# Kernel optimization log

Measured on AMD Instinct MI355X. Metric: run time of the kernel, lower is better.

## Reference

```python
import jax, jax.numpy as jnp
import numpy as np

N_NODES = 100000
N_EDGES = 1600000
FEAT = 64
HEADS = 8
OUT_C = 8  # per-head out channels; HEADS*OUT_C == FEAT
BATCH = 64
MAXLEN = 2048
NEG_SLOPE = 0.2  # PyG GATConv default


def setup_inputs() -> dict:
    key = jax.random.key(0)
    ks = jax.random.split(key, 8)
    x = jax.random.normal(ks[0], (N_NODES, FEAT), dtype=jnp.float32)
    edge_index = jax.random.randint(ks[1], (2, N_EDGES), 0, N_NODES, dtype=jnp.int64)
    traj_seqs = jax.random.randint(ks[2], (BATCH, MAXLEN), 0, N_NODES, dtype=jnp.int64)
    seq_lengths = jax.random.randint(ks[3], (BATCH,), 1, MAXLEN, dtype=jnp.int64)
    # GATConv parameters (glorot-ish init)
    W = jax.random.normal(ks[4], (FEAT, HEADS * OUT_C), dtype=jnp.float32) * (1.0 / np.sqrt(FEAT))
    att_src = jax.random.normal(ks[5], (HEADS, OUT_C), dtype=jnp.float32) * 0.1
    att_dst = jax.random.normal(ks[6], (HEADS, OUT_C), dtype=jnp.float32) * 0.1
    bias = jnp.zeros((HEADS * OUT_C,), dtype=jnp.float32)
    return {"x": x, "W": W, "att_src": att_src, "att_dst": att_dst, "bias": bias,
            "edge_index": edge_index, "traj_seqs": traj_seqs, "seq_lengths": seq_lengths}


def reference(x, W, att_src, att_dst, bias, edge_index, traj_seqs, seq_lengths):
    N = x.shape[0]
    # PyG GATConv adds self loops by default
    loop = jnp.arange(N, dtype=edge_index.dtype)
    src = jnp.concatenate([edge_index[0], loop])  # message source j
    dst = jnp.concatenate([edge_index[1], loop])  # message target i

    xw = (x @ W).reshape(N, HEADS, OUT_C)              # [N,H,C]
    a_src = jnp.sum(xw * att_src, axis=-1)             # [N,H]
    a_dst = jnp.sum(xw * att_dst, axis=-1)             # [N,H]

    # edge attention logits and segment softmax over incoming edges of dst
    e = jax.nn.leaky_relu(a_src[src] + a_dst[dst], NEG_SLOPE)   # [E,H]
    m = jax.ops.segment_max(e, dst, num_segments=N)             # [N,H]
    m = jnp.where(jnp.isfinite(m), m, 0.0)
    ex = jnp.exp(e - m[dst])
    denom = jax.ops.segment_sum(ex, dst, num_segments=N)        # [N,H] (>0 via self loops)
    alpha = ex / denom[dst]                                     # [E,H]

    msg = alpha[:, :, None] * xw[src]                           # [E,H,C]
    out = jax.ops.segment_sum(msg, dst, num_segments=N)         # [N,H,C]
    node_emb = jax.nn.relu(out.reshape(N, HEADS * OUT_C) + bias)

    # batched gather into padded [B, maxlen, F] tensor, zero past seq_lengths
    emb = node_emb[traj_seqs]                                   # [B,L,F]
    mask = jnp.arange(traj_seqs.shape[1])[None, :] < seq_lengths[:, None]
    emb = emb * mask[:, :, None].astype(emb.dtype)
    return emb, seq_lengths
```

## Files before the change

kernel.cpp:

```cpp
#include <hip/hip_runtime.h>
#include <hip/hip_bf16.h>
#include <hip/hip_fp8.h>
#include <hip/hip_fp16.h>

#define N_NODESC 100000
#define N_EDGESC 1600000
#define FEATC 64
#define HEADSC 8
#define BATCHC 64
#define MAXLENC 2048
#define NBUCK 500
#define BSZ 200
#define CAP 6144
#define P3_EDGES 8192
#define K1B 391

__device__ __forceinline__ float b2f(unsigned short u){
  union { unsigned u; float f; } c; c.u = ((unsigned)u) << 16; return c.f;
}
__device__ __forceinline__ unsigned short f2b(float f){
  union { float f; unsigned u; } c; c.f = f;
  unsigned r = c.u + 0x7fffu + ((c.u >> 16) & 1u);
  return (unsigned short)(r >> 16);
}
__device__ __forceinline__ int clampi(int v, int lo, int hi){
  return v < lo ? lo : (v > hi ? hi : v);
}
__device__ __forceinline__ void unpack8(uint4 v, float* o){
  o[0] = b2f((unsigned short)(v.x & 0xffff)); o[1] = b2f((unsigned short)(v.x >> 16));
  o[2] = b2f((unsigned short)(v.y & 0xffff)); o[3] = b2f((unsigned short)(v.y >> 16));
  o[4] = b2f((unsigned short)(v.z & 0xffff)); o[5] = b2f((unsigned short)(v.z >> 16));
  o[6] = b2f((unsigned short)(v.w & 0xffff)); o[7] = b2f((unsigned short)(v.w >> 16));
}
__device__ __forceinline__ float fp8tof(unsigned char b){
  __hip_fp8_e4m3 q; q.__x = (__hip_fp8_storage_t)b; return (float)q;
}

__global__ __launch_bounds__(256) void k_pre(
    const unsigned short* __restrict__ x, const unsigned short* __restrict__ W,
    const unsigned short* __restrict__ attS, const unsigned short* __restrict__ attD,
    const int* __restrict__ ei,
    unsigned char* __restrict__ xw8, __half* __restrict__ a_srch,
    float* __restrict__ a_dst, int* __restrict__ cc)
{
  __shared__ float Wsf[64 * 64];
  __shared__ float as_s[64];
  __shared__ float ad_s[64];
  __shared__ int hh[NBUCK];
  int t = threadIdx.x;

  if (blockIdx.x >= K1B) {
    for (int i = t; i < NBUCK; i += 256) hh[i] = 0;
    __syncthreads();
    int g = (blockIdx.x - K1B) * 256 + t;
    if (g < N_EDGESC / 4) {
      int4 d = ((const int4*)(ei + N_EDGESC))[g];
      atomicAdd(&hh[clampi(d.x, 0, N_NODESC - 1) / BSZ], 1);
      atomicAdd(&hh[clampi(d.y, 0, N_NODESC - 1) / BSZ], 1);
      atomicAdd(&hh[clampi(d.z, 0, N_NODESC - 1) / BSZ], 1);
      atomicAdd(&hh[clampi(d.w, 0, N_NODESC - 1) / BSZ], 1);
    }
    __syncthreads();
    for (int i = t; i < NBUCK; i += 256) if (hh[i]) atomicAdd(&cc[i], hh[i]);
    return;
  }

  for (int i = t; i < 4096; i += 256) Wsf[i] = b2f(W[i]);
  if (t < 64) { as_s[t] = b2f(attS[t]); ad_s[t] = b2f(attD[t]); }
  __syncthreads();

  int g    = t & 3;
  int slot = t >> 2;
  int n0 = blockIdx.x * 256 + slot * 4;

  float acc[4][16];
  #pragma unroll
  for (int j = 0; j < 4; j++)
    #pragma unroll
    for (int c = 0; c < 16; c++) acc[j][c] = 0.f;

  const float4* Ws4 = (const float4*)Wsf;
  for (int i = 0; i < 8; i++) {
    float xu[4][8];
    #pragma unroll
    for (int j = 0; j < 4; j++) {
      int n = n0 + j;
      uint4 v = make_uint4(0u,0u,0u,0u);
      if (n < N_NODESC) v = ((const uint4*)(x + (size_t)n * 64))[i];
      unpack8(v, xu[j]);
    }
    #pragma unroll
    for (int u = 0; u < 8; u++) {
      int k = i * 8 + u;
      float4 w0 = Ws4[k * 16 + g * 4 + 0];
      float4 w1 = Ws4[k * 16 + g * 4 + 1];
      float4 w2 = Ws4[k * 16 + g * 4 + 2];
      float4 w3 = Ws4[k * 16 + g * 4 + 3];
      #pragma unroll
      for (int j = 0; j < 4; j++) {
        float xk = xu[j][u];
        acc[j][ 0] += xk * w0.x; acc[j][ 1] += xk * w0.y;
        acc[j][ 2] += xk * w0.z; acc[j][ 3] += xk * w0.w;
        acc[j][ 4] += xk * w1.x; acc[j][ 5] += xk * w1.y;
        acc[j][ 6] += xk * w1.z; acc[j][ 7] += xk * w1.w;
        acc[j][ 8] += xk * w2.x; acc[j][ 9] += xk * w2.y;
        acc[j][10] += xk * w2.z; acc[j][11] += xk * w2.w;
        acc[j][12] += xk * w3.x; acc[j][13] += xk * w3.y;
        acc[j][14] += xk * w3.z; acc[j][15] += xk * w3.w;
      }
    }
  }

  #pragma unroll
  for (int j = 0; j < 4; j++) {
    int n = n0 + j;
    if (n >= N_NODESC) break;
    union { unsigned u[4]; unsigned char b[16]; } pk;
    #pragma unroll
    for (int c = 0; c < 16; c++)
      pk.b[c] = (unsigned char)__hip_fp8_e4m3(acc[j][c]).__x;
    uint4 o; o.x = pk.u[0]; o.y = pk.u[1]; o.z = pk.u[2]; o.w = pk.u[3];
    *((uint4*)(xw8 + (size_t)n * 64 + g * 16)) = o;

    #pragma unroll
    for (int hl = 0; hl < 2; hl++) {
      int h = g * 2 + hl;
      float sa = 0.f, sd = 0.f;
      #pragma unroll
      for (int c = 0; c < 8; c++) {
        sa += acc[j][hl * 8 + c] * as_s[h * 8 + c];
        sd += acc[j][hl * 8 + c] * ad_s[h * 8 + c];
      }
      a_srch[n * 8 + h] = __float2half(sa);
      a_dst[n * 8 + h] = sd;
    }
  }
}

__global__ __launch_bounds__(1024) void k_csort(const int* __restrict__ ei,
                                                const int* __restrict__ cc,
                                                int* __restrict__ gcur,
                                                unsigned* __restrict__ cs) {
  __shared__ int bst[512];
  __shared__ int h[NBUCK], lst[NBUCK], lcur[NBUCK], gb[NBUCK];
  __shared__ int sc[512];
  __shared__ unsigned sorted[P3_EDGES];
  __shared__ unsigned short sbk[P3_EDGES];
  int t = threadIdx.x;
  int base = blockIdx.x * P3_EDGES;
  for (int i = t; i < NBUCK; i += 1024) h[i] = 0;
  int myc = 0;
  if (t < 512) { myc = (t < NBUCK) ? cc[t] : 0; bst[t] = myc; }
  __syncthreads();
  for (int off = 1; off < 512; off <<= 1) {
    int v = 0;
    if (t < 512) { v = bst[t]; if (t >= off) v += bst[t - off]; }
    __syncthreads();
    if (t < 512) bst[t] = v;
    __syncthreads();
  }
  unsigned pk[8]; int bk[8];
  #pragma unroll
  for (int k = 0; k < 8; k++) {
    int idx = base + k * 1024 + t;
    bk[k] = -1;
    if (idx < N_EDGESC) {
      int s = clampi(ei[idx], 0, N_NODESC - 1);
      int d = clampi(ei[N_EDGESC + idx], 0, N_NODESC - 1);
      int b = d / BSZ;
      pk[k] = (unsigned)s | ((unsigned)(d - b * BSZ) << 17);
      bk[k] = b;
      atomicAdd(&h[b], 1);
    }
  }
  __syncthreads();
  if (t < 512) sc[t] = (t < NBUCK) ? h[t] : 0;
  __syncthreads();
  for (int off = 1; off < 512; off <<= 1) {
    int v = 0;
    if (t < 512) { v = sc[t]; if (t >= off) v += sc[t - off]; }
    __syncthreads();
    if (t < 512) sc[t] = v;
    __syncthreads();
  }
  if (t < NBUCK) {
    int ex = sc[t] - h[t];
    lst[t] = ex; lcur[t] = ex;
    if (h[t]) gb[t] = (bst[t] - myc) + atomicAdd(&gcur[t], h[t]);
  }
  __syncthreads();
  #pragma unroll
  for (int k = 0; k < 8; k++) if (bk[k] >= 0) {
    int p = atomicAdd(&lcur[bk[k]], 1);
    sorted[p] = pk[k];
    sbk[p] = (unsigned short)bk[k];
  }
  __syncthreads();
  int cnt = N_EDGESC - base; if (cnt > P3_EDGES) cnt = P3_EDGES;
  #pragma unroll
  for (int k = 0; k < 8; k++) {
    int i = k * 1024 + t;
    if (i < cnt) {
      int b = sbk[i];
      cs[gb[b] + (i - lst[b])] = sorted[i];
    }
  }
}

__global__ __launch_bounds__(1024) void k_aggf(
    const __half* __restrict__ a_srch, const float* __restrict__ a_dst,
    const unsigned char* __restrict__ xw8, const unsigned* __restrict__ cs,
    const int* __restrict__ cc,
    const unsigned short* __restrict__ bias, unsigned short* __restrict__ nembh)
{
  __shared__ int bsc[512];
  __shared__ int lcnt[256], loff[256], lcur[256];
  __shared__ int ssrc[CAP];
  __shared__ int sbase, scnt0;
  int t = threadIdx.x;
  int b = blockIdx.x;

  int myc = 0;
  if (t < 512) { myc = (t < NBUCK) ? cc[t] : 0; bsc[t] = myc; }
  __syncthreads();
  for (int off = 1; off < 512; off <<= 1) {
    int v = 0;
    if (t < 512) { v = bsc[t]; if (t >= off) v += bsc[t - off]; }
    __syncthreads();
    if (t < 512) bsc[t] = v;
    __syncthreads();
  }
  if (t == b) { sbase = bsc[t] - myc; scnt0 = myc; }
  if (t < 256) lcnt[t] = 0;
  __syncthreads();
  int base = sbase;
  int cnt  = scnt0;
  int scnt = cnt < CAP ? cnt : CAP;

  unsigned ce[6];
  #pragma unroll
  for (int j = 0; j < 6; j++) {
    int i = t + j * 1024;
    if (i < scnt) { ce[j] = cs[base + i]; atomicAdd(&lcnt[ce[j] >> 17], 1); }
  }
  __syncthreads();
  if (t < 256) loff[t] = lcnt[t];
  __syncthreads();
  for (int off = 1; off < 256; off <<= 1) {
    int v = 0;
    if (t < 256) { v = loff[t]; if (t >= off) v += loff[t - off]; }
    __syncthreads();
    if (t < 256) loff[t] = v;
    __syncthreads();
  }
  if (t < 256) { int ex = loff[t] - lcnt[t]; loff[t] = ex; lcur[t] = ex; }
  __syncthreads();
  #pragma unroll
  for (int j = 0; j < 6; j++) {
    int i = t + j * 1024;
    if (i < scnt) {
      int p = atomicAdd(&lcur[ce[j] >> 17], 1);
      ssrc[p] = (int)(ce[j] & 0x1FFFFu);
    }
  }
  __syncthreads();

  int wv = t >> 6;
  int l  = t & 63;
  int H  = l >> 3;
  int hw = l & 7;

  for (int dl = wv; dl < BSZ; dl += 16) {
    int dst = b * BSZ + dl;
    float adH = a_dst[dst * 8 + H];
    float zs  = __half2float(a_srch[dst * 8 + H]) + adH;
    float selfw = __expf(fmaxf(zs, 0.2f * zs));
    float acc = selfw * fp8tof(xw8[(size_t)dst * 64 + l]);
    float adW = a_dst[dst * 8 + hw];

    int beg = loff[dl];
    int end2 = beg + lcnt[dl];
    float lw = 0.f, lw2 = 0.f;

    for (int i = beg; i < end2; i += 8) {
      int idx = i + H;
      bool valid = idx < end2;
      int sv = ssrc[valid ? idx : end2 - 1];
      float av = __half2float(a_srch[sv * 8 + hw]);
      float z = av + adW;
      float w = __expf(fmaxf(z, 0.2f * z));
      w = valid ? w : 0.f;
      lw += w;
      #pragma unroll
      for (int e = 0; e < 8; e++) {
        int   se = __builtin_amdgcn_readlane(sv, e * 8);
        float wb = __shfl(w, (e << 3) + H, 64);
        float xv = fp8tof(xw8[(size_t)se * 64 + l]);
        acc += wb * xv;
      }
    }

    for (int i = CAP; i < cnt; i++) {
      unsigned e = cs[base + i];
      if ((int)(e >> 17) != dl) continue;
      int sv = (int)(e & 0x1FFFFu);
      float zz = __half2float(a_srch[sv * 8 + H]) + adH;
      float w = __expf(fmaxf(zz, 0.2f * zz));
      lw2 += w;
      acc += w * fp8tof(xw8[(size_t)sv * 64 + l]);
    }

    lw += __shfl_xor(lw, 8, 64);
    lw += __shfl_xor(lw, 16, 64);
    lw += __shfl_xor(lw, 32, 64);
    float denom = selfw + __shfl(lw, H, 64) + lw2;

    float v = acc / denom + b2f(bias[l]);
    nembh[(size_t)dst * 64 + l] = f2b(v > 0.f ? v : 0.f);
  }
}

__global__ __launch_bounds__(256) void k6_gather(
    const unsigned short* __restrict__ nembh, const int* __restrict__ traj,
    const int* __restrict__ lens, float* __restrict__ out)
{
  int gid = blockIdx.x * 256 + threadIdx.x;
  if (gid < BATCHC * MAXLENC * 16) {
    int b = gid >> 15;
    int rem = gid & 32767;
    int l = rem >> 4;
    int ch = rem & 15;
    int len = clampi(lens[b], 0, MAXLENC);
    float4 val = make_float4(0.f, 0.f, 0.f, 0.f);
    if (l < len) {
      int node = clampi(traj[b * MAXLENC + l], 0, N_NODESC - 1);
      uint2 q = ((const uint2*)nembh)[(size_t)node * 16 + ch];
      val = make_float4(b2f((unsigned short)(q.x & 0xffff)),
                        b2f((unsigned short)(q.x >> 16)),
                        b2f((unsigned short)(q.y & 0xffff)),
                        b2f((unsigned short)(q.y >> 16)));
    }
    ((float4*)out)[gid] = val;
  }
  if (gid < BATCHC) {
    out[(size_t)BATCHC * MAXLENC * FEATC + gid] = (float)lens[gid];
  }
}

extern "C" void kernel_launch(void* const* d_in, const int* in_sizes, int n_in,
                              void* d_out, int out_size, void* d_ws, size_t ws_size,
                              hipStream_t stream) {
  const unsigned short* x    = (const unsigned short*)d_in[0];
  const unsigned short* W    = (const unsigned short*)d_in[1];
  const unsigned short* attS = (const unsigned short*)d_in[2];
  const unsigned short* attD = (const unsigned short*)d_in[3];
  const unsigned short* bias = (const unsigned short*)d_in[4];
  const int* ei   = (const int*)d_in[5];
  const int* traj = (const int*)d_in[6];
  const int* lens = (const int*)d_in[7];
  float* out = (float*)d_out;

  float* F = (float*)d_ws;
  unsigned char* xw8 = (unsigned char*)d_ws;
  __half* a_srch = (__half*)(F + 3200000);
  float* a_dst   = F + 4000000;
  int* ccounts   = (int*)(F + 4900000);
  int* gcur      = (int*)(F + 4900000) + 512;
  unsigned* cs   = (unsigned*)(F + 5000000);
  unsigned short* nembh = (unsigned short*)(F + 6700000);

  hipMemsetAsync(ccounts, 0, 1024 * sizeof(int), stream);
  k_pre<<<K1B + (N_EDGESC / 4 + 255) / 256, 256, 0, stream>>>(
      x, W, attS, attD, ei, xw8, a_srch, a_dst, ccounts);
  k_csort<<<(N_EDGESC + P3_EDGES - 1) / P3_EDGES, 1024, 0, stream>>>(ei, ccounts, gcur, cs);
  k_aggf<<<NBUCK, 1024, 0, stream>>>(a_srch, a_dst, xw8, cs, ccounts, bias, nembh);
  k6_gather<<<(BATCHC * MAXLENC * 16 + 255) / 256, 256, 0, stream>>>(nembh, traj, lens, out);
}
```

Measured before the change: 200.4 us.

## Restructure GAT aggregation: 4-channel fp8 vector loads, edge-parallel lanes, software prefetch

After: 198.8 us. No clear change (-0.8%).

```diff
diff --git a/kernel.cpp b/kernel.cpp
--- a/kernel.cpp
+++ b/kernel.cpp
@@ -15,6 +15,8 @@
 #define P3_EDGES 8192
 #define K1B 391
 
+typedef float f32x2 __attribute__((ext_vector_type(2)));
+
 __device__ __forceinline__ float b2f(unsigned short u){
   union { unsigned u; float f; } c; c.u = ((unsigned)u) << 16; return c.f;
 }
@@ -34,6 +36,11 @@
 }
 __device__ __forceinline__ float fp8tof(unsigned char b){
   __hip_fp8_e4m3 q; q.__x = (__hip_fp8_storage_t)b; return (float)q;
+}
+__device__ __forceinline__ void cvt4(unsigned v, float* o){
+  f32x2 lo = __builtin_amdgcn_cvt_pk_f32_fp8((int)v, false);
+  f32x2 hi = __builtin_amdgcn_cvt_pk_f32_fp8((int)v, true);
+  o[0] = lo.x; o[1] = lo.y; o[2] = hi.x; o[3] = hi.y;
 }
 
 __global__ __launch_bounds__(256) void k_pre(
@@ -269,54 +276,104 @@
   int l  = t & 63;
   int H  = l >> 3;
   int hw = l & 7;
+  int k  = l & 15;
+  int g  = l >> 4;
+  int h2 = k >> 1;
+
+  int bp0 = ((g << 3) | h2) << 2;
+  int bp1 = (((g + 4) << 3) | h2) << 2;
+
+  uint2 bb = ((const uint2*)bias)[k];
+  float bs0 = b2f((unsigned short)(bb.x & 0xffff));
+  float bs1 = b2f((unsigned short)(bb.x >> 16));
+  float bs2 = b2f((unsigned short)(bb.y & 0xffff));
+  float bs3 = b2f((unsigned short)(bb.y >> 16));
 
   for (int dl = wv; dl < BSZ; dl += 16) {
     int dst = b * BSZ + dl;
-    float adH = a_dst[dst * 8 + H];
-    float zs  = __half2float(a_srch[dst * 8 + H]) + adH;
+    float adW = a_dst[dst * 8 + hw];
+    float adA = a_dst[dst * 8 + h2];
+    float zs  = __half2float(a_srch[dst * 8 + h2]) + adA;
     float selfw = __expf(fmaxf(zs, 0.2f * zs));
-    float acc = selfw * fp8tof(xw8[(size_t)dst * 64 + l]);
-    float adW = a_dst[dst * 8 + hw];
-
-    int beg = loff[dl];
-    int end2 = beg + lcnt[dl];
-    float lw = 0.f, lw2 = 0.f;
-
-    for (int i = beg; i < end2; i += 8) {
-      int idx = i + H;
-      bool valid = idx < end2;
-      int sv = ssrc[valid ? idx : end2 - 1];
-      float av = __half2float(a_srch[sv * 8 + hw]);
-      float z = av + adW;
-      float w = __expf(fmaxf(z, 0.2f * z));
-      w = valid ? w : 0.f;
-      lw += w;
-      #pragma unroll
-      for (int e = 0; e < 8; e++) {
-        int   se = __builtin_amdgcn_readlane(sv, e * 8);
-        float wb = __shfl(w, (e << 3) + H, 64);
-        float xv = fp8tof(xw8[(size_t)se * 64 + l]);
-        acc += wb * xv;
+
+    unsigned sd = *(const unsigned*)(xw8 + (size_t)dst * 64 + (k << 2));
+    float sx[4]; cvt4(sd, sx);
+    float sw = (g == 0) ? selfw : 0.f;
+    float a0 = sw * sx[0], a1 = sw * sx[1], a2 = sw * sx[2], a3 = sw * sx[3];
+
+    int beg  = loff[dl];
+    int deg  = lcnt[dl];
+    int end2 = beg + deg;
+    float lw = 0.f;
+
+    if (deg > 0) {
+      int last = end2 - 1;
+      int iw = beg + H; if (iw > last) iw = last;
+      float av = __half2float(a_srch[ssrc[iw] * 8 + hw]);
+      int e0 = beg + g;     if (e0 > last) e0 = last;
+      int e1 = beg + 4 + g; if (e1 > last) e1 = last;
+      unsigned d0 = *(const unsigned*)(xw8 + (size_t)ssrc[e0] * 64 + (k << 2));
+      unsigned d1 = *(const unsigned*)(xw8 + (size_t)ssrc[e1] * 64 + (k << 2));
+
+      for (int i = beg; i < end2; i += 8) {
+        float z = av + adW;
+        float w = __expf(fmaxf(z, 0.2f * z));
+        w = (i + H < end2) ? w : 0.f;
+        lw += w;
+        unsigned c0 = d0, c1 = d1;
+        int nx = i + 8;
+        if (nx < end2) {
+          int iw2 = nx + H; if (iw2 > last) iw2 = last;
+          av = __half2float(a_srch[ssrc[iw2] * 8 + hw]);
+          int f0 = nx + g;     if (f0 > last) f0 = last;
+          int f1 = nx + 4 + g; if (f1 > last) f1 = last;
+          d0 = *(const unsigned*)(xw8 + (size_t)ssrc[f0] * 64 + (k << 2));
+          d1 = *(const unsigned*)(xw8 + (size_t)ssrc[f1] * 64 + (k << 2));
+        }
+        int wi = __float_as_int(w);
+        float w0 = __int_as_float(__builtin_amdgcn_ds_bpermute(bp0, wi));
+        float w1 = __int_as_float(__builtin_amdgcn_ds_bpermute(bp1, wi));
+        float x0[4]; cvt4(c0, x0);
+        a0 += w0 * x0[0]; a1 += w0 * x0[1]; a2 += w0 * x0[2]; a3 += w0 * x0[3];
+        float x1[4]; cvt4(c1, x1);
+        a0 += w1 * x1[0]; a1 += w1 * x1[1]; a2 += w1 * x1[2]; a3 += w1 * x1[3];
       }
     }
 
+    a0 += __shfl_xor(a0, 16, 64); a0 += __shfl_xor(a0, 32, 64);
+    a1 += __shfl_xor(a1, 16, 64); a1 += __shfl_xor(a1, 32, 64);
+    a2 += __shfl_xor(a2, 16, 64); a2 += __shfl_xor(a2, 32, 64);
+    a3 += __shfl_xor(a3, 16, 64); a3 += __shfl_xor(a3, 32, 64);
+    lw += __shfl_xor(lw, 8, 64);
+    lw += __shfl_xor(lw, 16, 64);
+    lw += __shfl_xor(lw, 32, 64);
+    float dsum = __shfl(lw, h2, 64);
+
+    float lw2 = 0.f;
     for (int i = CAP; i < cnt; i++) {
       unsigned e = cs[base + i];
       if ((int)(e >> 17) != dl) continue;
       int sv = (int)(e & 0x1FFFFu);
-      float zz = __half2float(a_srch[sv * 8 + H]) + adH;
-      float w = __expf(fmaxf(zz, 0.2f * zz));
+      float z = __half2float(a_srch[sv * 8 + h2]) + adA;
+      float w = __expf(fmaxf(z, 0.2f * z));
       lw2 += w;
-      acc += w * fp8tof(xw8[(size_t)sv * 64 + l]);
-    }
-
-    lw += __shfl_xor(lw, 8, 64);
-    lw += __shfl_xor(lw, 16, 64);
-    lw += __shfl_xor(lw, 32, 64);
-    float denom = selfw + __shfl(lw, H, 64) + lw2;
-
-    float v = acc / denom + b2f(bias[l]);
-    nembh[(size_t)dst * 64 + l] = f2b(v > 0.f ? v : 0.f);
+      unsigned dv = *(const unsigned*)(xw8 + (size_t)sv * 64 + (k << 2));
+      float xo[4]; cvt4(dv, xo);
+      a0 += w * xo[0]; a1 += w * xo[1]; a2 += w * xo[2]; a3 += w * xo[3];
+    }
+
+    float denom = selfw + dsum + lw2;
+    if (l < 16) {
+      float inv = __builtin_amdgcn_rcpf(denom);
+      float v0 = a0 * inv + bs0; v0 = v0 > 0.f ? v0 : 0.f;
+      float v1 = a1 * inv + bs1; v1 = v1 > 0.f ? v1 : 0.f;
+      float v2 = a2 * inv + bs2; v2 = v2 > 0.f ? v2 : 0.f;
+      float v3 = a3 * inv + bs3; v3 = v3 > 0.f ? v3 : 0.f;
+      uint2 o;
+      o.x = (unsigned)f2b(v0) | ((unsigned)f2b(v1) << 16);
+      o.y = (unsigned)f2b(v2) | ((unsigned)f2b(v3) << 16);
+      ((uint2*)nembh)[(size_t)dst * 16 + k] = o;
+    }
   }
 }
 
```

## Remap aggregation lanes to edge-by-head with packed fp8 loads and prefetch

Applied to the files above, without the earlier changes.

Measured after the change: 203.6 us. No clear change (+1.6%).

```diff
diff --git a/kernel.cpp b/kernel.cpp
--- a/kernel.cpp
+++ b/kernel.cpp
@@ -15,6 +15,8 @@
 #define P3_EDGES 8192
 #define K1B 391
 
+typedef float f32x2 __attribute__((ext_vector_type(2)));
+
 __device__ __forceinline__ float b2f(unsigned short u){
   union { unsigned u; float f; } c; c.u = ((unsigned)u) << 16; return c.f;
 }
@@ -34,6 +36,11 @@
 }
 __device__ __forceinline__ float fp8tof(unsigned char b){
   __hip_fp8_e4m3 q; q.__x = (__hip_fp8_storage_t)b; return (float)q;
+}
+__device__ __forceinline__ void cvt4(unsigned v, float* o){
+  f32x2 lo = __builtin_amdgcn_cvt_pk_f32_fp8((int)v, false);
+  f32x2 hi = __builtin_amdgcn_cvt_pk_f32_fp8((int)v, true);
+  o[0] = lo.x; o[1] = lo.y; o[2] = hi.x; o[3] = hi.y;
 }
 
 __global__ __launch_bounds__(256) void k_pre(
@@ -207,7 +214,7 @@
   }
 }
 
-__global__ __launch_bounds__(1024) void k_aggf(
+__global__ __launch_bounds__(1024, 2) void k_aggf(
     const __half* __restrict__ a_srch, const float* __restrict__ a_dst,
     const unsigned char* __restrict__ xw8, const unsigned* __restrict__ cs,
     const int* __restrict__ cc,
@@ -215,7 +222,7 @@
 {
   __shared__ int bsc[512];
   __shared__ int lcnt[256], loff[256], lcur[256];
-  __shared__ int ssrc[CAP];
+  __shared__ int ssrc[CAP + 8];
   __shared__ int sbase, scnt0;
   int t = threadIdx.x;
   int b = blockIdx.x;
@@ -263,60 +270,110 @@
       ssrc[p] = (int)(ce[j] & 0x1FFFFu);
     }
   }
+  for (int i = scnt + t; i < CAP + 8; i += 1024) ssrc[i] = 0;
   __syncthreads();
 
   int wv = t >> 6;
   int l  = t & 63;
-  int H  = l >> 3;
-  int hw = l & 7;
+  int e  = l >> 3;
+  int h  = l & 7;
+
+  uint4 bb = ((const uint4*)bias)[h];
 
   for (int dl = wv; dl < BSZ; dl += 16) {
     int dst = b * BSZ + dl;
-    float adH = a_dst[dst * 8 + H];
-    float zs  = __half2float(a_srch[dst * 8 + H]) + adH;
+    float adH = a_dst[dst * 8 + h];
+    float zs  = __half2float(a_srch[dst * 8 + h]) + adH;
     float selfw = __expf(fmaxf(zs, 0.2f * zs));
-    float acc = selfw * fp8tof(xw8[(size_t)dst * 64 + l]);
-    float adW = a_dst[dst * 8 + hw];
-
-    int beg = loff[dl];
-    int end2 = beg + lcnt[dl];
-    float lw = 0.f, lw2 = 0.f;
+
+    uint2 sd = *(const uint2*)(xw8 + ((unsigned)dst << 6) + (h << 3));
+    float sx0[4], sx1[4]; cvt4(sd.x, sx0); cvt4(sd.y, sx1);
+    float sw = (e == 0) ? selfw : 0.f;
+    float a0 = sw * sx0[0], a1 = sw * sx0[1], a2 = sw * sx0[2], a3 = sw * sx0[3];
+    float a4 = sw * sx1[0], a5 = sw * sx1[1], a6 = sw * sx1[2], a7 = sw * sx1[3];
+    float lwl = sw;
+
+    int beg  = loff[dl];
+    int deg  = lcnt[dl];
+    int end2 = beg + deg;
+
+    float av0 = 0.f, av1 = 0.f;
+    uint2 d0 = make_uint2(0u, 0u), d1 = make_uint2(0u, 0u);
+    if (deg > 0) {
+      int s0 = ssrc[beg + e];
+      av0 = __half2float(a_srch[s0 * 8 + h]);
+      d0  = *(const uint2*)(xw8 + ((unsigned)s0 << 6) + (h << 3));
+    }
+    if (deg > 8) {
+      int s1 = ssrc[beg + 8 + e];
+      av1 = __half2float(a_srch[s1 * 8 + h]);
+      d1  = *(const uint2*)(xw8 + ((unsigned)s1 << 6) + (h << 3));
+    }
 
     for (int i = beg; i < end2; i += 8) {
-      int idx = i + H;
-      bool valid = idx < end2;
-      int sv = ssrc[valid ? idx : end2 - 1];
-      float av = __half2float(a_srch[sv * 8 + hw]);
-      float z = av + adW;
+      float av = av0; uint2 dd = d0;
+      av0 = av1; d0 = d1;
+      int nx = i + 16;
+      if (nx < end2) {
+        int sn = ssrc[nx + e];
+        av1 = __half2float(a_srch[sn * 8 + h]);
+        d1  = *(const uint2*)(xw8 + ((unsigned)sn << 6) + (h << 3));
+      }
+      float z = av + adH;
       float w = __expf(fmaxf(z, 0.2f * z));
-      w = valid ? w : 0.f;
-      lw += w;
-      #pragma unroll
-      for (int e = 0; e < 8; e++) {
-        int   se = __builtin_amdgcn_readlane(sv, e * 8);
-        float wb = __shfl(w, (e << 3) + H, 64);
-        float xv = fp8tof(xw8[(size_t)se * 64 + l]);
-        acc += wb * xv;
-      }
-    }
-
+      w = (i + e < end2) ? w : 0.f;
+      lwl += w;
+      float x0[4], x1[4];
+      cvt4(dd.x, x0); cvt4(dd.y, x1);
+      a0 += w * x0[0]; a1 += w * x0[1]; a2 += w * x0[2]; a3 += w * x0[3];
+      a4 += w * x1[0]; a5 += w * x1[1]; a6 += w * x1[2]; a7 += w * x1[3];
+    }
+
+    a0 += __shfl_xor(a0, 8, 64); a0 += __shfl_xor(a0, 16, 64); a0 += __shfl_xor(a0, 32, 64);
+    a1 += __shfl_xor(a1, 8, 64); a1 += __shfl_xor(a1, 16, 64); a1 += __shfl_xor(a1, 32, 64);
+    a2 += __shfl_xor(a2, 8, 64); a2 += __shfl_xor(a2, 16, 64); a2 += __shfl_xor(a2, 32, 64);
+    a3 += __shfl_xor(a3, 8, 64); a3 += __shfl_xor(a3, 16, 64); a3 += __shfl_xor(a3, 32, 64);
+    a4 += __shfl_xor(a4, 8, 64); a4 += __shfl_xor(a4, 16, 64); a4 += __shfl_xor(a4, 32, 64);
+    a5 += __shfl_xor(a5, 8, 64); a5 += __shfl_xor(a5, 16, 64); a5 += __shfl_xor(a5, 32, 64);
+    a6 += __shfl_xor(a6, 8, 64); a6 += __shfl_xor(a6, 16, 64); a6 += __shfl_xor(a6, 32, 64);
+    a7 += __shfl_xor(a7, 8, 64); a7 += __shfl_xor(a7, 16, 64); a7 += __shfl_xor(a7, 32, 64);
+    lwl += __shfl_xor(lwl, 8, 64); lwl += __shfl_xor(lwl, 16, 64); lwl += __shfl_xor(lwl, 32, 64);
+
+    float lw2 = 0.f;
     for (int i = CAP; i < cnt; i++) {
-      unsigned e = cs[base + i];
-      if ((int)(e >> 17) != dl) continue;
-      int sv = (int)(e & 0x1FFFFu);
-      float zz = __half2float(a_srch[sv * 8 + H]) + adH;
-      float w = __expf(fmaxf(zz, 0.2f * zz));
+      unsigned ev = cs[base + i];
+      if ((int)(ev >> 17) != dl) continue;
+      int sv = (int)(ev & 0x1FFFFu);
+      float z = __half2float(a_srch[sv * 8 + h]) + adH;
+      float w = __expf(fmaxf(z, 0.2f * z));
       lw2 += w;
-      acc += w * fp8tof(xw8[(size_t)sv * 64 + l]);
-    }
-
-    lw += __shfl_xor(lw, 8, 64);
-    lw += __shfl_xor(lw, 16, 64);
-    lw += __shfl_xor(lw, 32, 64);
-    float denom = selfw + __shfl(lw, H, 64) + lw2;
-
-    float v = acc / denom + b2f(bias[l]);
-    nembh[(size_t)dst * 64 + l] = f2b(v > 0.f ? v : 0.f);
+      uint2 dv = *(const uint2*)(xw8 + ((unsigned)sv << 6) + (h << 3));
+      float y0[4], y1[4]; cvt4(dv.x, y0); cvt4(dv.y, y1);
+      a0 += w * y0[0]; a1 += w * y0[1]; a2 += w * y0[2]; a3 += w * y0[3];
+      a4 += w * y1[0]; a5 += w * y1[1]; a6 += w * y1[2]; a7 += w * y1[3];
+    }
+
+    if (l < 8) {
+      float inv = __builtin_amdgcn_rcpf(lwl + lw2);
+      float v0 = a0 * inv + b2f((unsigned short)(bb.x & 0xffff));
+      float v1 = a1 * inv + b2f((unsigned short)(bb.x >> 16));
+      float v2 = a2 * inv + b2f((unsigned short)(bb.y & 0xffff));
+      float v3 = a3 * inv + b2f((unsigned short)(bb.y >> 16));
+      float v4 = a4 * inv + b2f((unsigned short)(bb.z & 0xffff));
+      float v5 = a5 * inv + b2f((unsigned short)(bb.z >> 16));
+      float v6 = a6 * inv + b2f((unsigned short)(bb.w & 0xffff));
+      float v7 = a7 * inv + b2f((unsigned short)(bb.w >> 16));
+      v0 = v0 > 0.f ? v0 : 0.f; v1 = v1 > 0.f ? v1 : 0.f;
+      v2 = v2 > 0.f ? v2 : 0.f; v3 = v3 > 0.f ? v3 : 0.f;
+      v4 = v4 > 0.f ? v4 : 0.f; v5 = v5 > 0.f ? v5 : 0.f;
+      v6 = v6 > 0.f ? v6 : 0.f; v7 = v7 > 0.f ? v7 : 0.f;
+      uint4 o;
+      o.x = (unsigned)f2b(v0) | ((unsigned)f2b(v1) << 16);
+      o.y = (unsigned)f2b(v2) | ((unsigned)f2b(v3) << 16);
+      o.z = (unsigned)f2b(v4) | ((unsigned)f2b(v5) << 16);
+      o.w = (unsigned)f2b(v6) | ((unsigned)f2b(v7) << 16);
+      ((uint4*)nembh)[(size_t)dst * 8 + l] = o;
+    }
   }
 }
 
```

## Aggregate edges via shared-memory atomics instead of per-destination local sort

Applied to the files above, without the earlier changes.

Result: slower. 762.3 us (+280.4%).

```diff
diff --git a/kernel.cpp b/kernel.cpp
--- a/kernel.cpp
+++ b/kernel.cpp
@@ -11,9 +11,10 @@
 #define MAXLENC 2048
 #define NBUCK 500
 #define BSZ 200
-#define CAP 6144
 #define P3_EDGES 8192
 #define K1B 391
+
+typedef float f32x2 __attribute__((ext_vector_type(2)));
 
 __device__ __forceinline__ float b2f(unsigned short u){
   union { unsigned u; float f; } c; c.u = ((unsigned)u) << 16; return c.f;
@@ -32,8 +33,10 @@
   o[4] = b2f((unsigned short)(v.z & 0xffff)); o[5] = b2f((unsigned short)(v.z >> 16));
   o[6] = b2f((unsigned short)(v.w & 0xffff)); o[7] = b2f((unsigned short)(v.w >> 16));
 }
-__device__ __forceinline__ float fp8tof(unsigned char b){
-  __hip_fp8_e4m3 q; q.__x = (__hip_fp8_storage_t)b; return (float)q;
+__device__ __forceinline__ void cvt4(unsigned v, float* o){
+  f32x2 lo = __builtin_amdgcn_cvt_pk_f32_fp8((int)v, false);
+  f32x2 hi = __builtin_amdgcn_cvt_pk_f32_fp8((int)v, true);
+  o[0] = lo.x; o[1] = lo.y; o[2] = hi.x; o[3] = hi.y;
 }
 
 __global__ __launch_bounds__(256) void k_pre(
@@ -140,7 +143,8 @@
 __global__ __launch_bounds__(1024) void k_csort(const int* __restrict__ ei,
                                                 const int* __restrict__ cc,
                                                 int* __restrict__ gcur,
-                                                unsigned* __restrict__ cs) {
+                                                unsigned* __restrict__ cs,
+                                                int* __restrict__ boff) {
   __shared__ int bst[512];
   __shared__ int h[NBUCK], lst[NBUCK], lcur[NBUCK], gb[NBUCK];
   __shared__ int sc[512];
@@ -159,6 +163,7 @@
     if (t < 512) bst[t] = v;
     __syncthreads();
   }
+  if (blockIdx.x == 0 && t < NBUCK) boff[t] = bst[t] - myc;
   unsigned pk[8]; int bk[8];
   #pragma unroll
   for (int k = 0; k < 8; k++) {
@@ -207,116 +212,83 @@
   }
 }
 
-__global__ __launch_bounds__(1024) void k_aggf(
+__global__ __launch_bounds__(1024, 2) void k_aggf(
     const __half* __restrict__ a_srch, const float* __restrict__ a_dst,
     const unsigned char* __restrict__ xw8, const unsigned* __restrict__ cs,
-    const int* __restrict__ cc,
+    const int* __restrict__ cc, const int* __restrict__ boff,
     const unsigned short* __restrict__ bias, unsigned short* __restrict__ nembh)
 {
-  __shared__ int bsc[512];
-  __shared__ int lcnt[256], loff[256], lcur[256];
-  __shared__ int ssrc[CAP];
-  __shared__ int sbase, scnt0;
+  __shared__ float sacc[BSZ * 68];
+  __shared__ float sden[BSZ * 9];
+  __shared__ float sad[BSZ * 9];
   int t = threadIdx.x;
   int b = blockIdx.x;
-
-  int myc = 0;
-  if (t < 512) { myc = (t < NBUCK) ? cc[t] : 0; bsc[t] = myc; }
-  __syncthreads();
-  for (int off = 1; off < 512; off <<= 1) {
-    int v = 0;
-    if (t < 512) { v = bsc[t]; if (t >= off) v += bsc[t - off]; }
-    __syncthreads();
-    if (t < 512) bsc[t] = v;
-    __syncthreads();
-  }
-  if (t == b) { sbase = bsc[t] - myc; scnt0 = myc; }
-  if (t < 256) lcnt[t] = 0;
-  __syncthreads();
-  int base = sbase;
-  int cnt  = scnt0;
-  int scnt = cnt < CAP ? cnt : CAP;
-
-  unsigned ce[6];
-  #pragma unroll
-  for (int j = 0; j < 6; j++) {
-    int i = t + j * 1024;
-    if (i < scnt) { ce[j] = cs[base + i]; atomicAdd(&lcnt[ce[j] >> 17], 1); }
-  }
-  __syncthreads();
-  if (t < 256) loff[t] = lcnt[t];
-  __syncthreads();
-  for (int off = 1; off < 256; off <<= 1) {
-    int v = 0;
-    if (t < 256) { v = loff[t]; if (t >= off) v += loff[t - off]; }
-    __syncthreads();
-    if (t < 256) loff[t] = v;
-    __syncthreads();
-  }
-  if (t < 256) { int ex = loff[t] - lcnt[t]; loff[t] = ex; lcur[t] = ex; }
-  __syncthreads();
-  #pragma unroll
-  for (int j = 0; j < 6; j++) {
-    int i = t + j * 1024;
-    if (i < scnt) {
-      int p = atomicAdd(&lcur[ce[j] >> 17], 1);
-      ssrc[p] = (int)(ce[j] & 0x1FFFFu);
-    }
-  }
-  __syncthreads();
-
-  int wv = t >> 6;
-  int l  = t & 63;
-  int H  = l >> 3;
-  int hw = l & 7;
-
-  for (int dl = wv; dl < BSZ; dl += 16) {
+  int base = boff[b];
+  int cnt  = cc[b];
+
+  for (int i = t; i < BSZ * 8; i += 1024) {
+    int dl = i >> 3, h = i & 7;
     int dst = b * BSZ + dl;
-    float adH = a_dst[dst * 8 + H];
-    float zs  = __half2float(a_srch[dst * 8 + H]) + adH;
-    float selfw = __expf(fmaxf(zs, 0.2f * zs));
-    float acc = selfw * fp8tof(xw8[(size_t)dst * 64 + l]);
-    float adW = a_dst[dst * 8 + hw];
-
-    int beg = loff[dl];
-    int end2 = beg + lcnt[dl];
-    float lw = 0.f, lw2 = 0.f;
-
-    for (int i = beg; i < end2; i += 8) {
-      int idx = i + H;
-      bool valid = idx < end2;
-      int sv = ssrc[valid ? idx : end2 - 1];
-      float av = __half2float(a_srch[sv * 8 + hw]);
-      float z = av + adW;
-      float w = __expf(fmaxf(z, 0.2f * z));
-      w = valid ? w : 0.f;
-      lw += w;
-      #pragma unroll
-      for (int e = 0; e < 8; e++) {
-        int   se = __builtin_amdgcn_readlane(sv, e * 8);
-        float wb = __shfl(w, (e << 3) + H, 64);
-        float xv = fp8tof(xw8[(size_t)se * 64 + l]);
-        acc += wb * xv;
-      }
-    }
-
-    for (int i = CAP; i < cnt; i++) {
-      unsigned e = cs[base + i];
-      if ((int)(e >> 17) != dl) continue;
-      int sv = (int)(e & 0x1FFFFu);
-      float zz = __half2float(a_srch[sv * 8 + H]) + adH;
-      float w = __expf(fmaxf(zz, 0.2f * zz));
-      lw2 += w;
-      acc += w * fp8tof(xw8[(size_t)sv * 64 + l]);
-    }
-
-    lw += __shfl_xor(lw, 8, 64);
-    lw += __shfl_xor(lw, 16, 64);
-    lw += __shfl_xor(lw, 32, 64);
-    float denom = selfw + __shfl(lw, H, 64) + lw2;
-
-    float v = acc / denom + b2f(bias[l]);
-    nembh[(size_t)dst * 64 + l] = f2b(v > 0.f ? v : 0.f);
+    float adv = a_dst[dst * 8 + h];
+    float sa  = __half2float(a_srch[dst * 8 + h]);
+    sad[dl * 9 + h] = adv;
+    float zs = sa + adv;
+    sden[dl * 9 + h] = __expf(fmaxf(zs, 0.2f * zs));
+  }
+  __syncthreads();
+  for (int i = t; i < BSZ * 16; i += 1024) {
+    int dl = i >> 4, q = i & 15, h = q >> 1;
+    int dst = b * BSZ + dl;
+    unsigned xr = *(const unsigned*)(xw8 + ((unsigned)dst << 6) + (q << 2));
+    float xv[4]; cvt4(xr, xv);
+    float sw = sden[dl * 9 + h];
+    int ab = dl * 68 + q * 4;
+    sacc[ab + 0] = sw * xv[0]; sacc[ab + 1] = sw * xv[1];
+    sacc[ab + 2] = sw * xv[2]; sacc[ab + 3] = sw * xv[3];
+  }
+  __syncthreads();
+
+  int wv = t >> 6, l = t & 63, e = l >> 3, h = l & 7;
+  int ngroups = (cnt + 7) >> 3;
+  #pragma unroll 2
+  for (int gp = wv; gp < ngroups; gp += 16) {
+    int ei_ = gp * 8 + e;
+    bool valid = ei_ < cnt;
+    int rd = valid ? ei_ : (cnt - 1);
+    unsigned pk = cs[base + rd];
+    int src = (int)(pk & 0x1FFFFu);
+    int dl  = (int)(pk >> 17);
+    float av = __half2float(a_srch[src * 8 + h]);
+    uint2 xr = *(const uint2*)(xw8 + ((unsigned)src << 6) + (h << 3));
+    float z = av + sad[dl * 9 + h];
+    float w = __expf(fmaxf(z, 0.2f * z));
+    if (!valid) w = 0.f;
+    atomicAdd(&sden[dl * 9 + h], w);
+    float x0[4], x1[4]; cvt4(xr.x, x0); cvt4(xr.y, x1);
+    int ab = dl * 68 + h * 8;
+    atomicAdd(&sacc[ab + 0], w * x0[0]); atomicAdd(&sacc[ab + 1], w * x0[1]);
+    atomicAdd(&sacc[ab + 2], w * x0[2]); atomicAdd(&sacc[ab + 3], w * x0[3]);
+    atomicAdd(&sacc[ab + 4], w * x1[0]); atomicAdd(&sacc[ab + 5], w * x1[1]);
+    atomicAdd(&sacc[ab + 6], w * x1[2]); atomicAdd(&sacc[ab + 7], w * x1[3]);
+  }
+  __syncthreads();
+
+  for (int i = t; i < BSZ * 16; i += 1024) {
+    int dl = i >> 4, q = i & 15, h = q >> 1;
+    int dst = b * BSZ + dl;
+    float4 a = *(float4*)&sacc[dl * 68 + q * 4];
+    float inv = __builtin_amdgcn_rcpf(sden[dl * 9 + h]);
+    uint2 bb = ((const uint2*)bias)[q];
+    float v0 = a.x * inv + b2f((unsigned short)(bb.x & 0xffff));
+    float v1 = a.y * inv + b2f((unsigned short)(bb.x >> 16));
+    float v2 = a.z * inv + b2f((unsigned short)(bb.y & 0xffff));
+    float v3 = a.w * inv + b2f((unsigned short)(bb.y >> 16));
+    v0 = fmaxf(v0, 0.f); v1 = fmaxf(v1, 0.f);
+    v2 = fmaxf(v2, 0.f); v3 = fmaxf(v3, 0.f);
+    uint2 o;
+    o.x = (unsigned)f2b(v0) | ((unsigned)f2b(v1) << 16);
+    o.y = (unsigned)f2b(v2) | ((unsigned)f2b(v3) << 16);
+    ((uint2*)nembh)[(size_t)dst * 16 + q] = o;
   }
 }
 
@@ -366,13 +338,14 @@
   float* a_dst   = F + 4000000;
   int* ccounts   = (int*)(F + 4900000);
   int* gcur      = (int*)(F + 4900000) + 512;
+  int* boff      = (int*)(F + 4900000) + 1024;
   unsigned* cs   = (unsigned*)(F + 5000000);
   unsigned short* nembh = (unsigned short*)(F + 6700000);
 
   hipMemsetAsync(ccounts, 0, 1024 * sizeof(int), stream);
   k_pre<<<K1B + (N_EDGESC / 4 + 255) / 256, 256, 0, stream>>>(
       x, W, attS, attD, ei, xw8, a_srch, a_dst, ccounts);
-  k_csort<<<(N_EDGESC + P3_EDGES - 1) / P3_EDGES, 1024, 0, stream>>>(ei, ccounts, gcur, cs);
-  k_aggf<<<NBUCK, 1024, 0, stream>>>(a_srch, a_dst, xw8, cs, ccounts, bias, nembh);
+  k_csort<<<(N_EDGESC + P3_EDGES - 1) / P3_EDGES, 1024, 0, stream>>>(ei, ccounts, gcur, cs, boff);
+  k_aggf<<<NBUCK, 1024, 0, stream>>>(a_srch, a_dst, xw8, cs, ccounts, boff, bias, nembh);
   k6_gather<<<(BATCHC * MAXLENC * 16 + 255) / 256, 256, 0, stream>>>(nembh, traj, lens, out);
 }
```
